# Kernel tuning notes

Measured on AMD Instinct MI355X. Metric: run time of the kernel, lower is better.

Reference implementation:

```python
import jax, jax.numpy as jnp
import numpy as np

B, V, K = 128, 128000, 20
_SAMPLING_EPS = 1e-5


def setup_inputs() -> dict:
    key = jax.random.key(0)
    k1, k2, k3 = jax.random.split(key, 3)
    logits = jax.random.normal(k1, (B, V), dtype=jnp.float32)
    temp = jax.random.uniform(k2, (B,), dtype=jnp.float32, minval=0.2, maxval=1.5)
    # every 4th sequence is greedy (temperature < eps)
    temp = jnp.where(jnp.arange(B) % 4 == 0, 0.0, temp)
    # uniform noise in (0,1); exponential noise is q = -log(u)
    u = jax.random.uniform(k3, (B, V), dtype=jnp.float32, minval=1e-7, maxval=1.0)
    return {"logits": logits, "temp": temp, "u": u, "max_num_logprobs": K}


def reference(logits, temp, u, max_num_logprobs):
    # apply_temperature: greedy rows (temp < eps) use temp=1.0
    t = jnp.where(temp < _SAMPLING_EPS, 1.0, temp)
    scaled = logits.astype(jnp.float32) / t[:, None]          # [B, V]
    probs = jax.nn.softmax(scaled, axis=-1)                    # [B, V]
    # greedy sample
    greedy = jnp.argmax(probs, axis=1)                         # [B]
    # random sample via exponential-race (Gumbel-max equivalent): argmax(probs / Exp(1))
    q = -jnp.log(u)                                            # Exp(1) noise
    random_sampled = jnp.argmax(probs / q, axis=1)             # [B]
    sampled = jnp.where(temp < _SAMPLING_EPS, greedy, random_sampled)
    # top-k logprobs
    logprobs = jax.nn.log_softmax(scaled, axis=-1)             # [B, V]
    topk_logprobs, topk_indices = jax.lax.top_k(logprobs, max_num_logprobs)
    return sampled, topk_logprobs, topk_indices
```

## Files before the change

### kernel.cpp

```cpp
#include <hip/hip_runtime.h>
#include <stdint.h>


#define KMAX 20
#define SAMPLING_EPS 1e-5f
#define TAU 3.0f
#define CPB 64

static __device__ __forceinline__ unsigned int ord32(float v) {
    unsigned int u = __float_as_uint(v);
    return u ^ ((unsigned int)((int)u >> 31) | 0x80000000u);
}
static __device__ __forceinline__ float unord32(unsigned int x) {
    unsigned int u = (x & 0x80000000u) ? (x ^ 0x80000000u) : ~x;
    return __uint_as_float(u);
}
static __device__ __forceinline__ unsigned long long shflxor64(unsigned long long v, int off) {
    int lo = __shfl_xor((int)(unsigned int)v, off, 64);
    int hi = __shfl_xor((int)(unsigned int)(v >> 32), off, 64);
    return ((unsigned long long)(unsigned int)hi << 32) | (unsigned int)lo;
}

static __device__ __forceinline__ float gumbel_exact(float x, float inv_t, float uu, float wm) {
    const float q = (uu > 0.984375f) ? -log1pf(-wm) : -__logf(uu);
    return x * inv_t - __logf(q);
}

__global__ __launch_bounds__(256, 8) void k1_partials(
        const float* __restrict__ logits, const float* __restrict__ u,
        const float* __restrict__ temp,
        unsigned int* __restrict__ wrec,
        unsigned int* __restrict__ cntbuf,
        uint2* __restrict__ candbuf,
        int V, int nsplit) {
    __shared__ int cnt;
    __shared__ uint2 cand[CPB];
    const int b = blockIdx.x;
    const int r = b / nsplit;
    const int sp = b - r * nsplit;
    const int t = threadIdx.x;
    const int lane = t & 63;
    const int w = t >> 6;
    if (t == 0) cnt = 0;
    __syncthreads();

    const float traw = temp[r];
    const bool greedy = traw < SAMPLING_EPS;
    const float inv_t = greedy ? 1.0f : (1.0f / traw);

    const int nf4 = V >> 2;
    const int per = (nf4 + nsplit - 1) / nsplit;
    const int f0 = sp * per;
    const int f1 = min(f0 + per, nf4);

    const float4* __restrict__ l4 = (const float4*)(logits + (size_t)r * V);
    const float4* __restrict__ u4 = (const float4*)(u + (size_t)r * V);

    float s = 0.0f;
    float gv = -INFINITY;
    int gcol = 0;

    if (greedy) {
        for (int f = f0 + t; f < f1; f += 256) {
            const float4 lv = l4[f];
            const int colb = f << 2;
            #pragma unroll
            for (int j = 0; j < 4; ++j) {
                const float x = (&lv.x)[j];
                s += __expf(x * inv_t);
                if (x >= TAU) {
                    const int idx = atomicAdd(&cnt, 1);
                    if (idx < CPB) cand[idx] = make_uint2(__float_as_uint(x), (unsigned)(colb + j));
                }
            }
        }
    } else {
        int f = f0 + t;
        if (f < f1) {
            const float4 lv = l4[f];
            const float4 uv = u4[f];
            const int colb = f << 2;
            #pragma unroll
            for (int j = 0; j < 4; ++j) {
                const float x = (&lv.x)[j];
                s += __expf(x * inv_t);
                const float uu = (&uv.x)[j];
                const float g = gumbel_exact(x, inv_t, uu, 1.0f - uu);
                if (g > gv) { gv = g; gcol = colb + j; }
                if (x >= TAU) {
                    const int idx = atomicAdd(&cnt, 1);
                    if (idx < CPB) cand[idx] = make_uint2(__float_as_uint(x), (unsigned)(colb + j));
                }
            }
        }
        float gmax = gv;
        #pragma unroll
        for (int off = 1; off < 64; off <<= 1) gmax = fmaxf(gmax, __shfl_xor(gmax, off, 64));
        float gvs = gmax - 1e-5f;

        for (f += 256; f < f1; f += 256) {
            const float4 lv = l4[f];
            const float4 uv = u4[f];
            const int colb = f << 2;
            #pragma unroll
            for (int j = 0; j < 4; ++j) {
                const float x = (&lv.x)[j];
                const float arg = x * inv_t;
                s += __expf(arg);
                const float uu = (&uv.x)[j];
                const float wm = 1.0f - uu;
                const int ew = 127 - (int)(__float_as_uint(wm) >> 23);
                const float gub = fmaf((float)ew, 0.69314718f, arg);
                if (gub > gvs) {
                    const float g = gumbel_exact(x, inv_t, uu, wm);
                    if (g > gv) { gv = g; gcol = colb + j; gvs = g - 1e-5f; }
                }
                if (x >= TAU) {
                    const int idx = atomicAdd(&cnt, 1);
                    if (idx < CPB) cand[idx] = make_uint2(__float_as_uint(x), (unsigned)(colb + j));
                }
            }
        }
    }

    #pragma unroll
    for (int off = 1; off < 64; off <<= 1) s += __shfl_xor(s, off, 64);
    unsigned long long gk = greedy ? 0ull
        : (((unsigned long long)ord32(gv) << 32) | (unsigned int)~(unsigned int)gcol);
    #pragma unroll
    for (int off = 1; off < 64; off <<= 1) {
        const unsigned long long o = shflxor64(gk, off);
        gk = (o > gk) ? o : gk;
    }
    if (lane == 0) {
        unsigned int* rp = wrec + (size_t)(b * 4 + w) * 4;
        rp[0] = __float_as_uint(s);
        rp[1] = __float_as_uint(unord32((unsigned int)(gk >> 32)));
        rp[2] = ~(unsigned int)gk;
    }
    __syncthreads();
    const int c = cnt;
    if (t == 0) cntbuf[b] = (unsigned)c;
    if (t < min(c, CPB)) candbuf[(size_t)b * CPB + t] = cand[t];
}

__global__ __launch_bounds__(64) void k2_finalize(
        const unsigned int* __restrict__ wrec, const unsigned int* __restrict__ cntbuf,
        const uint2* __restrict__ candbuf, const float* __restrict__ logits,
        const float* __restrict__ temp, float* __restrict__ out,
        int B, int V, int K, int nsplit) {
    __shared__ unsigned long long kbuf[512];
    const int r = blockIdx.x;
    const int lane = threadIdx.x;
    const int NW = nsplit * 4;

    const float traw = temp[r];
    const bool greedy = traw < SAMPLING_EPS;
    const float tt = greedy ? 1.0f : traw;

    float s = 0.0f;
    unsigned long long gk = 0ull;
    if (lane < NW) {
        const unsigned int* rp = wrec + (size_t)(r * NW + lane) * 4;
        s = __uint_as_float(rp[0]);
        gk = ((unsigned long long)ord32(__uint_as_float(rp[1])) << 32) | (unsigned int)~rp[2];
    }
    #pragma unroll
    for (int off = 1; off < 64; off <<= 1) s += __shfl_xor(s, off, 64);
    #pragma unroll
    for (int off = 1; off < 64; off <<= 1) {
        const unsigned long long o = shflxor64(gk, off);
        gk = (o > gk) ? o : gk;
    }
    const float lS = logf(s);

    const int cnt_raw = (lane < nsplit) ? (int)cntbuf[r * nsplit + lane] : 0;
    const int cntc = min(cnt_raw, CPB);
    const bool ovf = __ballot(cnt_raw > CPB) != 0ull;
    int incl = cntc;
    #pragma unroll
    for (int d = 1; d < 64; d <<= 1) {
        const int o = __shfl_up(incl, d, 64);
        if (lane >= d) incl += o;
    }
    const int T = __shfl(incl, 63, 64);
    const int off0 = incl - cntc;

    unsigned long long keys[8];
    #pragma unroll
    for (int jj = 0; jj < 8; ++jj) keys[jj] = 0ull;

    if (!ovf && T >= K && T <= 512) {
        if (lane < nsplit) {
            const uint2* cb = candbuf + (size_t)(r * nsplit + lane) * CPB;
            for (int i = 0; i < cntc; ++i) {
                const uint2 e = cb[i];
                kbuf[off0 + i] = ((unsigned long long)ord32(__uint_as_float(e.x)) << 32)
                               | (unsigned int)~e.y;
            }
        }
        __syncthreads();
        #pragma unroll
        for (int jj = 0; jj < 8; ++jj) {
            const int idx = lane + 64 * jj;
            if (idx < T) keys[jj] = kbuf[idx];
        }
    } else {
        unsigned long long mykey = ((unsigned long long)0x007FFFFFu) << 32;
        unsigned long long minkey = mykey;
        float vmin = -INFINITY;
        const float* lr = logits + (size_t)r * V;
        for (int base = 0; base < V; base += 64) {
            const int i = base + lane;
            const float x = (i < V) ? lr[i] : -INFINITY;
            unsigned long long cm = __ballot((i < V) && (x >= vmin));
            while (cm) {
                const int src = (int)__builtin_ctzll(cm);
                cm &= cm - 1;
                const float cv = __shfl(x, src, 64);
                const int cc = __shfl(i, src, 64);
                const unsigned long long ck =
                    ((unsigned long long)ord32(cv) << 32) | (unsigned int)~(unsigned int)cc;
                if (ck > minkey) {
                    const bool own = (lane < K) && (mykey == minkey);
                    const unsigned long long om = __ballot(own);
                    if (lane == (int)__builtin_ctzll(om)) mykey = ck;
                    unsigned long long mk = (lane < K) ? mykey : ~0ull;
                    #pragma unroll
                    for (int o2 = 1; o2 < 64; o2 <<= 1) {
                        const unsigned long long o = shflxor64(mk, o2);
                        mk = (o < mk) ? o : mk;
                    }
                    minkey = mk;
                    vmin = unord32((unsigned int)(mk >> 32));
                }
            }
        }
        keys[0] = (lane < K) ? mykey : 0ull;
    }

    float* out_s  = out;
    float* out_lp = out + B;
    float* out_ix = out + B + (size_t)B * K;

    unsigned int top1 = 0;
    for (int k = 0; k < K; ++k) {
        unsigned long long loc = keys[0];
        #pragma unroll
        for (int jj = 1; jj < 8; ++jj) loc = (keys[jj] > loc) ? keys[jj] : loc;
        #pragma unroll
        for (int off = 1; off < 64; off <<= 1) {
            const unsigned long long o = shflxor64(loc, off);
            loc = (o > loc) ? o : loc;
        }
        #pragma unroll
        for (int jj = 0; jj < 8; ++jj) if (keys[jj] == loc) keys[jj] = 0ull;
        if (lane == 0) {
            const unsigned int col = ~(unsigned int)loc;
            const float v = unord32((unsigned int)(loc >> 32));
            out_lp[(size_t)r * K + k] = v / tt - lS;
            out_ix[(size_t)r * K + k] = (float)col;
            if (k == 0) top1 = col;
        }
    }
    if (lane == 0) {
        out_s[r] = (float)(greedy ? top1 : (~(unsigned int)gk));
    }
}

extern "C" void kernel_launch(void* const* d_in, const int* in_sizes, int n_in,
                              void* d_out, int out_size, void* d_ws, size_t ws_size,
                              hipStream_t stream) {
    const float* logits = (const float*)d_in[0];
    const float* temp   = (const float*)d_in[1];
    const float* u      = (const float*)d_in[2];
    const int B = in_sizes[1];
    const int V = in_sizes[0] / B;
    int K = (out_size - B) / (2 * B);
    if (K > KMAX) K = KMAX;
    if (K < 1) K = 1;

    int nsplit = 16;
    while (nsplit > 1 && (size_t)B * nsplit * 580 > ws_size) nsplit >>= 1;
    const int blocks = B * nsplit;

    unsigned int* wrec   = (unsigned int*)d_ws;
    unsigned int* cntbuf = wrec + (size_t)blocks * 16;
    uint2*        candbf = (uint2*)(cntbuf + blocks);

    k1_partials<<<dim3(blocks), dim3(256), 0, stream>>>(
        logits, u, temp, wrec, cntbuf, candbf, V, nsplit);
    k2_finalize<<<dim3(B), dim3(64), 0, stream>>>(
        wrec, cntbuf, candbf, logits, temp, (float*)d_out, B, V, K, nsplit);
}
```

Baseline: 161.5 us.

## Batch four float4 loads per iteration and parallelize candidate gathering in finalize

Result: slower. 176.2 us (+9.2%).

```diff
diff --git a/kernel.cpp b/kernel.cpp
--- a/kernel.cpp
+++ b/kernel.cpp
@@ -52,6 +52,7 @@
     const int per = (nf4 + nsplit - 1) / nsplit;
     const int f0 = sp * per;
     const int f1 = min(f0 + per, nf4);
+    const int f1m = f1 - 1;
 
     const float4* __restrict__ l4 = (const float4*)(logits + (size_t)r * V);
     const float4* __restrict__ u4 = (const float4*)(u + (size_t)r * V);
@@ -61,28 +62,40 @@
     int gcol = 0;
 
     if (greedy) {
-        for (int f = f0 + t; f < f1; f += 256) {
-            const float4 lv = l4[f];
-            const int colb = f << 2;
+        for (int fb = f0 + t; fb < f1; fb += 1024) {
+            float4 lv[4];
+            int fc[4];
+            #pragma unroll
+            for (int i = 0; i < 4; ++i) {
+                fc[i] = min(fb + (i << 8), f1m);
+                lv[i] = l4[fc[i]];
+            }
+            #pragma unroll
+            for (int i = 0; i < 4; ++i) {
+                const bool act = (fb + (i << 8)) < f1;
+                const int colb = fc[i] << 2;
+                #pragma unroll
+                for (int j = 0; j < 4; ++j) {
+                    const float x = act ? (&lv[i].x)[j] : -INFINITY;
+                    s += __expf(x * inv_t);
+                    if (x >= TAU) {
+                        const int idx = atomicAdd(&cnt, 1);
+                        if (idx < CPB) cand[idx] = make_uint2(__float_as_uint(x), (unsigned)(colb + j));
+                    }
+                }
+            }
+        }
+    } else {
+        {
+            const int f = f0 + t;
+            const int fc = min(f, f1m);
+            const bool act = f < f1;
+            const float4 lv = l4[fc];
+            const float4 uv = u4[fc];
+            const int colb = fc << 2;
             #pragma unroll
             for (int j = 0; j < 4; ++j) {
-                const float x = (&lv.x)[j];
-                s += __expf(x * inv_t);
-                if (x >= TAU) {
-                    const int idx = atomicAdd(&cnt, 1);
-                    if (idx < CPB) cand[idx] = make_uint2(__float_as_uint(x), (unsigned)(colb + j));
-                }
-            }
-        }
-    } else {
-        int f = f0 + t;
-        if (f < f1) {
-            const float4 lv = l4[f];
-            const float4 uv = u4[f];
-            const int colb = f << 2;
-            #pragma unroll
-            for (int j = 0; j < 4; ++j) {
-                const float x = (&lv.x)[j];
+                const float x = act ? (&lv.x)[j] : -INFINITY;
                 s += __expf(x * inv_t);
                 const float uu = (&uv.x)[j];
                 const float g = gumbel_exact(x, inv_t, uu, 1.0f - uu);
@@ -98,26 +111,37 @@
         for (int off = 1; off < 64; off <<= 1) gmax = fmaxf(gmax, __shfl_xor(gmax, off, 64));
         float gvs = gmax - 1e-5f;
 
-        for (f += 256; f < f1; f += 256) {
-            const float4 lv = l4[f];
-            const float4 uv = u4[f];
-            const int colb = f << 2;
-            #pragma unroll
-            for (int j = 0; j < 4; ++j) {
-                const float x = (&lv.x)[j];
-                const float arg = x * inv_t;
-                s += __expf(arg);
-                const float uu = (&uv.x)[j];
-                const float wm = 1.0f - uu;
-                const int ew = 127 - (int)(__float_as_uint(wm) >> 23);
-                const float gub = fmaf((float)ew, 0.69314718f, arg);
-                if (gub > gvs) {
-                    const float g = gumbel_exact(x, inv_t, uu, wm);
-                    if (g > gv) { gv = g; gcol = colb + j; gvs = g - 1e-5f; }
-                }
-                if (x >= TAU) {
-                    const int idx = atomicAdd(&cnt, 1);
-                    if (idx < CPB) cand[idx] = make_uint2(__float_as_uint(x), (unsigned)(colb + j));
+        for (int fb = f0 + t + 256; fb < f1; fb += 1024) {
+            float4 lv[4], uv[4];
+            int fc[4];
+            #pragma unroll
+            for (int i = 0; i < 4; ++i) {
+                fc[i] = min(fb + (i << 8), f1m);
+                lv[i] = l4[fc[i]];
+            }
+            #pragma unroll
+            for (int i = 0; i < 4; ++i) uv[i] = u4[fc[i]];
+            #pragma unroll
+            for (int i = 0; i < 4; ++i) {
+                const bool act = (fb + (i << 8)) < f1;
+                const int colb = fc[i] << 2;
+                #pragma unroll
+                for (int j = 0; j < 4; ++j) {
+                    const float x = act ? (&lv[i].x)[j] : -INFINITY;
+                    const float arg = x * inv_t;
+                    s += __expf(arg);
+                    const float uu = (&uv[i].x)[j];
+                    const float wm = 1.0f - uu;
+                    const int ew = 127 - (int)(__float_as_uint(wm) >> 23);
+                    const float gub = fmaf((float)ew, 0.69314718f, arg);
+                    if (gub > gvs) {
+                        const float g = gumbel_exact(x, inv_t, uu, wm);
+                        if (g > gv) { gv = g; gcol = colb + j; gvs = g - 1e-5f; }
+                    }
+                    if (x >= TAU) {
+                        const int idx = atomicAdd(&cnt, 1);
+                        if (idx < CPB) cand[idx] = make_uint2(__float_as_uint(x), (unsigned)(colb + j));
+                    }
                 }
             }
         }
@@ -137,6 +161,7 @@
         rp[0] = __float_as_uint(s);
         rp[1] = __float_as_uint(unord32((unsigned int)(gk >> 32)));
         rp[2] = ~(unsigned int)gk;
+        rp[3] = 0u;
     }
     __syncthreads();
     const int c = cnt;
@@ -161,9 +186,9 @@
     float s = 0.0f;
     unsigned long long gk = 0ull;
     if (lane < NW) {
-        const unsigned int* rp = wrec + (size_t)(r * NW + lane) * 4;
-        s = __uint_as_float(rp[0]);
-        gk = ((unsigned long long)ord32(__uint_as_float(rp[1])) << 32) | (unsigned int)~rp[2];
+        const uint4 rv = ((const uint4*)wrec)[(size_t)r * NW + lane];
+        s = __uint_as_float(rv.x);
+        gk = ((unsigned long long)ord32(__uint_as_float(rv.y)) << 32) | (unsigned int)~rv.z;
     }
     #pragma unroll
     for (int off = 1; off < 64; off <<= 1) s += __shfl_xor(s, off, 64);
@@ -175,31 +200,37 @@
     const float lS = logf(s);
 
     const int cnt_raw = (lane < nsplit) ? (int)cntbuf[r * nsplit + lane] : 0;
-    const int cntc = min(cnt_raw, CPB);
+    const int myc = min(cnt_raw, CPB);
     const bool ovf = __ballot(cnt_raw > CPB) != 0ull;
-    int incl = cntc;
+    int incl = myc;
     #pragma unroll
     for (int d = 1; d < 64; d <<= 1) {
         const int o = __shfl_up(incl, d, 64);
         if (lane >= d) incl += o;
     }
     const int T = __shfl(incl, 63, 64);
-    const int off0 = incl - cntc;
+
+    const int rec = lane >> 2;
+    const int sl0 = lane & 3;
+    if (rec < nsplit) {
+        const int cbase = __shfl(incl - myc, rec, 64);
+        const int ccnt  = __shfl(myc, rec, 64);
+        const uint2* cb = candbuf + (size_t)(r * nsplit + rec) * CPB;
+        for (int i = sl0; i < ccnt; i += 4) {
+            if (cbase + i < 512) {
+                const uint2 e = cb[i];
+                kbuf[cbase + i] = ((unsigned long long)ord32(__uint_as_float(e.x)) << 32)
+                                | (unsigned int)~e.y;
+            }
+        }
+    }
+    __syncthreads();
 
     unsigned long long keys[8];
     #pragma unroll
     for (int jj = 0; jj < 8; ++jj) keys[jj] = 0ull;
 
     if (!ovf && T >= K && T <= 512) {
-        if (lane < nsplit) {
-            const uint2* cb = candbuf + (size_t)(r * nsplit + lane) * CPB;
-            for (int i = 0; i < cntc; ++i) {
-                const uint2 e = cb[i];
-                kbuf[off0 + i] = ((unsigned long long)ord32(__uint_as_float(e.x)) << 32)
-                               | (unsigned int)~e.y;
-            }
-        }
-        __syncthreads();
         #pragma unroll
         for (int jj = 0; jj < 8; ++jj) {
             const int idx = lane + 64 * jj;
```
